# Kernel optimization log

Measured on AMD Instinct MI355X. Metric: run time of the kernel, lower is better.

The kernel has to match this reference:

```python
import jax, jax.numpy as jnp
import numpy as np

WS = 8   # window_size
SS = 4   # shift_size
NH = 8   # num_heads
EPS = 1e-5

def _ln(x, w, b):
    m = jnp.mean(x, axis=-1, keepdims=True)
    v = jnp.var(x, axis=-1, keepdims=True)
    return (x - m) * jax.lax.rsqrt(v + EPS) * w + b

def setup_inputs() -> dict:
    key = jax.random.key(0)
    ks = jax.random.split(key, 6)
    E = 256
    s = 0.02
    return {
        "x": jax.random.normal(ks[0], (8, E, 128, 128), jnp.float32),
        "ln1_w": jnp.ones((E,), jnp.float32),
        "ln1_b": jnp.zeros((E,), jnp.float32),
        "in_proj_w": jax.random.normal(ks[1], (3 * E, E), jnp.float32) * s,
        "in_proj_b": jnp.zeros((3 * E,), jnp.float32),
        "out_proj_w": jax.random.normal(ks[2], (E, E), jnp.float32) * s,
        "out_proj_b": jnp.zeros((E,), jnp.float32),
        "ln2_w": jnp.ones((E,), jnp.float32),
        "ln2_b": jnp.zeros((E,), jnp.float32),
        "mlp_w1": jax.random.normal(ks[3], (4 * E, E), jnp.float32) * s,
        "mlp_b1": jnp.zeros((4 * E,), jnp.float32),
        "mlp_w2": jax.random.normal(ks[4], (E, 4 * E), jnp.float32) * s,
        "mlp_b2": jnp.zeros((E,), jnp.float32),
    }

def reference(x, ln1_w, ln1_b, in_proj_w, in_proj_b, out_proj_w, out_proj_b,
              ln2_w, ln2_b, mlp_w1, mlp_b1, mlp_w2, mlp_b2):
    B, C, H, W = x.shape
    dh = C // NH
    # NCHW -> NHWC, cyclic shift
    xh = jnp.transpose(x, (0, 2, 3, 1))
    xh = jnp.roll(xh, (-SS, -SS), axis=(1, 2))
    # window partition: [B*nWh*nWw, WS*WS, C]
    nWh, nWw = H // WS, W // WS
    win = xh.reshape(B, nWh, WS, nWw, WS, C).transpose(0, 1, 3, 2, 4, 5)
    win = win.reshape(-1, WS * WS, C)
    h = _ln(win, ln1_w, ln1_b)
    qkv = h @ in_proj_w.T + in_proj_b                       # [N, 64, 3C]
    q, k, v = jnp.split(qkv, 3, axis=-1)
    N, T, _ = q.shape
    q = q.reshape(N, T, NH, dh).transpose(0, 2, 1, 3)       # [N, NH, T, dh]
    k = k.reshape(N, T, NH, dh).transpose(0, 2, 1, 3)
    v = v.reshape(N, T, NH, dh).transpose(0, 2, 1, 3)
    scores = jnp.einsum('nhqd,nhkd->nhqk', q, k) / jnp.sqrt(jnp.float32(dh))
    attn = jax.nn.softmax(scores, axis=-1)
    o = jnp.einsum('nhqk,nhkd->nhqd', attn, v)
    o = o.transpose(0, 2, 1, 3).reshape(N, T, C)
    o = o @ out_proj_w.T + out_proj_b
    win = win + o
    # MLP
    h2 = _ln(win, ln2_w, ln2_b)
    m = jax.nn.gelu(h2 @ mlp_w1.T + mlp_b1, approximate=False)
    m = m @ mlp_w2.T + mlp_b2
    win = win + m
    # window reverse + unshift
    xh = win.reshape(B, nWh, nWw, WS, WS, C).transpose(0, 1, 3, 2, 4, 5)
    xh = xh.reshape(B, H, W, C)
    xh = jnp.roll(xh, (SS, SS), axis=(1, 2))
    return jnp.transpose(xh, (0, 3, 1, 2))
```

## Files before the change

### kernel.cpp

```cpp
#include <hip/hip_runtime.h>
#include <math.h>


#define LDH 264
#define LDS_S 40

typedef __attribute__((ext_vector_type(8))) short bf16x8;
typedef __attribute__((ext_vector_type(4))) short bf16x4;
typedef __attribute__((ext_vector_type(4))) float f32x4;

#define WF(wf, tile, KT, kt, ln) (*(const bf16x8*)&(wf)[((((tile)*(KT)) + (kt))*64 + (ln))*8])
#define FRAG(basep, ttile, KT, kt, l) (*(const bf16x8*)&(basep)[((((ttile)*(KT)) + (kt))*64 + (l))*8])

static __device__ __forceinline__ float bf2f(short s){
  union { unsigned u; float f; } cv;
  cv.u = ((unsigned)(unsigned short)s) << 16;
  return cv.f;
}
static __device__ __forceinline__ short f2bf(float f){
  __bf16 h = (__bf16)f;
  union { __bf16 b; short s; } cv; cv.b = h;
  return cv.s;
}
static __device__ __forceinline__ unsigned pk2bf(float lo, float hi){
  return (unsigned)(unsigned short)f2bf(lo) | ((unsigned)(unsigned short)f2bf(hi) << 16);
}
static __device__ __forceinline__ float gelu_f(float x){
  const float x2 = x * x;
  const float u  = x * fmaf(0.0713537014f, x2, 1.5957691216f);
  const float e  = __expf(u);
  const float r  = __builtin_amdgcn_rcpf(e + 1.f);
  return x * (1.f - r);
}

__global__ void wpack_kernel(const float* __restrict__ src, short* __restrict__ dst,
                             int K){
  const int t8 = blockIdx.x * 256 + threadIdx.x;
  const int e0 = t8 * 8;
  const int l   = (e0 >> 3) & 63;
  const int blk = e0 >> 9;
  const int KT  = K >> 5;
  const int kt   = blk % KT;
  const int tile = blk / KT;
  const int row = tile*16 + (l & 15);
  const int kb  = kt*32 + (l >> 4)*8;
  const float* s = src + row*K + kb;
  bf16x8 o;
  #pragma unroll
  for (int e=0;e<8;++e) o[e] = f2bf(s[e]);
  *(bf16x8*)&dst[e0] = o;
}

#define K1_OFF_WV  33792
#define K1_OFF_RED 74752
#define K1_SMEM    76800

__global__ __launch_bounds__(256, 2)
void swin_attn_kernel(const float* __restrict__ x,
                      const float* __restrict__ ln1w, const float* __restrict__ ln1b,
                      const float* __restrict__ inb,  const float* __restrict__ outb,
                      const short* __restrict__ wqkv, const short* __restrict__ wout,
                      short* __restrict__ win2T)
{
  __shared__ char smem[K1_SMEM];
  short* shf    = (short*)smem;
  short* sh_o   = (short*)smem;
  short* xsh    = (short*)(smem + K1_OFF_WV);
  float* red_s  = (float*)(smem + K1_OFF_RED);
  float* red_q2 = red_s + 256;

  const int tid = threadIdx.x;
  const int wv  = tid >> 6;
  const int ln  = tid & 63;
  const int rowa = ln & 15;
  const int kg   = ln >> 4;

  short* slotA = (short*)(smem + K1_OFF_WV) + wv*5120;
  short* slotB = slotA + 2560;

  const int bid = blockIdx.x;
  const int wi  = ((bid & 7) << 8) | (bid >> 3);
  const int b  = wi >> 8;
  const int wh = (wi >> 4) & 15;
  const int ww = wi & 15;

  const int hh = (wh*8 + (ln >> 3) + 4) & 127;
  const int wc = (ww*8 + (ln & 7) + 4) & 127;
  const int offhw = hh*128 + wc;
  const int xbase = b << 22;

  unsigned xpk[32];
  {
    const int cbeg = wv*64;
    float vals[64];
    float s = 0.f, sq = 0.f;
    #pragma unroll
    for (int j = 0; j < 64; ++j){
      float v = x[xbase + ((cbeg + j) << 14) + offhw];
      vals[j] = v; s += v; sq += v*v;
    }
    #pragma unroll
    for (int p = 0; p < 32; ++p)
      xpk[p] = pk2bf(vals[2*p], vals[2*p+1]);
    red_s[cbeg + ln]  = s;
    red_q2[cbeg + ln] = sq;
    __syncthreads();
    float sum = red_s[ln] + red_s[64+ln] + red_s[128+ln] + red_s[192+ln];
    float ssq = red_q2[ln] + red_q2[64+ln] + red_q2[128+ln] + red_q2[192+ln];
    float mean = sum * 0.00390625f;
    float var  = ssq * 0.00390625f - mean*mean;
    float rstd = rsqrtf(var + 1e-5f);
    const int ttile = ln >> 4;
    #pragma unroll
    for (int kl=0;kl<2;++kl){
      const int kt = wv*2 + kl;
      #pragma unroll
      for (int kgw=0;kgw<4;++kgw){
        bf16x8 pkv;
        #pragma unroll
        for (int e=0;e<8;++e){
          const int j = kl*32 + kgw*8 + e;
          const int c = cbeg + j;
          pkv[e] = f2bf((vals[j] - mean) * rstd * ln1w[c] + ln1b[c]);
        }
        *(bf16x8*)&shf[(((ttile*8 + kt)*64) + kgw*16 + (ln & 15))*8] = pkv;
      }
    }
  }
  __syncthreads();

  const float scale = 0.1767766952966369f;
  f32x4 oacc[4][4];
  #pragma unroll
  for (int mt=0;mt<4;++mt)
    #pragma unroll
    for (int j=0;j<4;++j)
      oacc[mt][j] = (f32x4){0.f,0.f,0.f,0.f};

  const int s0 = ((kg & 1) << 5) + rowa;

  #pragma unroll
  for (int hd = 0; hd < 2; ++hd){
    const int hc = (2*wv + hd) * 32;
    const int tq = (2*wv + hd) * 2;

    {
      f32x4 aq[4][2], ak[4][2];
      #pragma unroll
      for (int mt=0;mt<4;++mt){
        aq[mt][0]=(f32x4){0,0,0,0}; aq[mt][1]=(f32x4){0,0,0,0};
        ak[mt][0]=(f32x4){0,0,0,0}; ak[mt][1]=(f32x4){0,0,0,0};
      }
      #pragma unroll
      for (int kt=0;kt<8;++kt){
        bf16x8 av[4], bq[2], bk[2];
        #pragma unroll
        for (int mt=0;mt<4;++mt)
          av[mt] = FRAG(shf, mt, 8, kt, ln);
        #pragma unroll
        for (int nt=0;nt<2;++nt){
          bq[nt] = WF(wqkv, tq + nt,      8, kt, ln);
          bk[nt] = WF(wqkv, 16 + tq + nt, 8, kt, ln);
        }
        #pragma unroll
        for (int mt=0;mt<4;++mt)
          #pragma unroll
          for (int nt=0;nt<2;++nt){
            aq[mt][nt] = __builtin_amdgcn_mfma_f32_16x16x32_bf16(av[mt], bq[nt], aq[mt][nt], 0, 0, 0);
            ak[mt][nt] = __builtin_amdgcn_mfma_f32_16x16x32_bf16(av[mt], bk[nt], ak[mt][nt], 0, 0, 0);
          }
      }
      #pragma unroll
      for (int nt=0;nt<2;++nt){
        const float biasq = inb[hc + nt*16 + rowa];
        const float biask = inb[256 + hc + nt*16 + rowa];
        #pragma unroll
        for (int mt=0;mt<4;++mt)
          #pragma unroll
          for (int i=0;i<4;++i){
            slotA[(mt*16 + kg*4 + i)*LDS_S + nt*16 + rowa] = f2bf(aq[mt][nt][i] + biasq);
            slotB[(mt*16 + kg*4 + i)*LDS_S + nt*16 + rowa] = f2bf(ak[mt][nt][i] + biask);
          }
      }
    }

    f32x4 sacc[4][4];
    #pragma unroll
    for (int mt=0;mt<4;++mt)
      #pragma unroll
      for (int nt=0;nt<4;++nt)
        sacc[mt][nt] = (f32x4){0.f,0.f,0.f,0.f};
    {
      bf16x8 aq[4], bk[4];
      #pragma unroll
      for (int mt=0;mt<4;++mt)
        aq[mt] = *(const bf16x8*)&slotA[(mt*16+rowa)*LDS_S + kg*8];
      #pragma unroll
      for (int nt=0;nt<4;++nt)
        bk[nt] = *(const bf16x8*)&slotB[(nt*16+rowa)*LDS_S + kg*8];
      __builtin_amdgcn_s_setprio(1);
      #pragma unroll
      for (int mt=0;mt<4;++mt)
        #pragma unroll
        for (int nt=0;nt<4;++nt)
          sacc[mt][nt] = __builtin_amdgcn_mfma_f32_16x16x32_bf16(aq[mt], bk[nt], sacc[mt][nt], 0, 0, 0);
      __builtin_amdgcn_s_setprio(0);
    }

    unsigned pkv[4][2][2];
    {
      f32x4 accv[4][2];
      #pragma unroll
      for (int mt=0;mt<4;++mt){ accv[mt][0]=(f32x4){0,0,0,0}; accv[mt][1]=(f32x4){0,0,0,0}; }
      #pragma unroll
      for (int kt=0;kt<8;++kt){
        bf16x8 av[4], bw[2];
        #pragma unroll
        for (int mt=0;mt<4;++mt)
          av[mt] = FRAG(shf, mt, 8, kt, ln);
        #pragma unroll
        for (int nt=0;nt<2;++nt)
          bw[nt] = WF(wqkv, 32 + tq + nt, 8, kt, ln);
        #pragma unroll
        for (int mt=0;mt<4;++mt)
          #pragma unroll
          for (int nt=0;nt<2;++nt)
            accv[mt][nt] = __builtin_amdgcn_mfma_f32_16x16x32_bf16(av[mt], bw[nt], accv[mt][nt], 0, 0, 0);
      }
      #pragma unroll
      for (int nt=0;nt<2;++nt){
        const float bias = inb[512 + hc + nt*16 + rowa];
        #pragma unroll
        for (int mt=0;mt<4;++mt){
          pkv[mt][nt][0] = pk2bf(accv[mt][nt][0] + bias, accv[mt][nt][1] + bias);
          pkv[mt][nt][1] = pk2bf(accv[mt][nt][2] + bias, accv[mt][nt][3] + bias);
        }
      }
    }

    #pragma unroll
    for (int mt=0;mt<4;++mt){
      #pragma unroll
      for (int i=0;i<4;++i){
        float v0 = sacc[mt][0][i]*scale;
        float v1 = sacc[mt][1][i]*scale;
        float v2 = sacc[mt][2][i]*scale;
        float v3 = sacc[mt][3][i]*scale;
        float mx = fmaxf(fmaxf(v0,v1), fmaxf(v2,v3));
        #pragma unroll
        for (int d=1; d<16; d<<=1) mx = fmaxf(mx, __shfl_xor(mx, d, 64));
        v0 = __expf(v0-mx); v1 = __expf(v1-mx); v2 = __expf(v2-mx); v3 = __expf(v3-mx);
        float sm = v0+v1+v2+v3;
        #pragma unroll
        for (int d=1; d<16; d<<=1) sm += __shfl_xor(sm, d, 64);
        const float inv = 1.f / sm;
        sacc[mt][0][i] = v0*inv; sacc[mt][1][i] = v1*inv;
        sacc[mt][2][i] = v2*inv; sacc[mt][3][i] = v3*inv;
      }
    }

    #pragma unroll
    for (int ck=0; ck<2; ++ck){
      #pragma unroll
      for (int ntl=0; ntl<2; ++ntl)
        #pragma unroll
        for (int mt=0;mt<4;++mt)
          #pragma unroll
          for (int i=0;i<4;++i)
            slotA[(mt*16 + kg*4 + i)*LDS_S + ntl*16 + rowa] = f2bf(sacc[mt][2*ck+ntl][i]);
      bf16x8 bv[2];
      #pragma unroll
      for (int nt=0;nt<2;++nt){
        union { unsigned u[4]; bf16x8 v; } bb;
        #pragma unroll
        for (int dh2=0; dh2<2; ++dh2){
          #pragma unroll
          for (int w=0; w<2; ++w){
            const unsigned pe = (unsigned)__shfl((int)pkv[2*ck    ][nt][w], s0 + dh2*16);
            const unsigned po = (unsigned)__shfl((int)pkv[2*ck + 1][nt][w], s0 + dh2*16);
            bb.u[dh2*2 + w] = (kg & 2) ? po : pe;
          }
        }
        bv[nt] = bb.v;
      }
      bf16x8 ap[4];
      #pragma unroll
      for (int mt=0;mt<4;++mt)
        ap[mt] = *(const bf16x8*)&slotA[(mt*16+rowa)*LDS_S + kg*8];
      __builtin_amdgcn_s_setprio(1);
      #pragma unroll
      for (int mt=0;mt<4;++mt)
        #pragma unroll
        for (int nt=0;nt<2;++nt)
          oacc[mt][hd*2+nt] = __builtin_amdgcn_mfma_f32_16x16x32_bf16(ap[mt], bv[nt], oacc[mt][hd*2+nt], 0, 0, 0);
      __builtin_amdgcn_s_setprio(0);
    }
  }

  __syncthreads();

  #pragma unroll
  for (int j=0;j<4;++j){
    const int col = wv*64 + j*16 + rowa;
    #pragma unroll
    for (int mt=0;mt<4;++mt)
      #pragma unroll
      for (int i=0;i<4;++i)
        sh_o[(mt*16 + kg*4 + i)*LDH + col] = f2bf(oacc[mt][j][i]);
  }
  {
    const int cbeg = wv*64;
    #pragma unroll
    for (int q=0;q<8;++q){
      bf16x8 pk;
      #pragma unroll
      for (int e=0;e<4;++e){
        const unsigned w = xpk[q*4+e];
        pk[2*e]   = (short)(w & 0xffffu);
        pk[2*e+1] = (short)(w >> 16);
      }
      *(bf16x8*)&xsh[ln*LDH + cbeg + q*8] = pk;
    }
  }
  __syncthreads();

  {
    f32x4 acc[4][4];
    #pragma unroll
    for (int c0=0;c0<4;++c0)
      #pragma unroll
      for (int t0=0;t0<4;++t0)
        acc[c0][t0] = (f32x4){0.f,0.f,0.f,0.f};
    for (int kt=0; kt<8; ++kt){
      bf16x8 aw[4], bo[4];
      #pragma unroll
      for (int c0=0;c0<4;++c0)
        aw[c0] = WF(wout, wv*4 + c0, 8, kt, ln);
      #pragma unroll
      for (int t0=0;t0<4;++t0)
        bo[t0] = *(const bf16x8*)&sh_o[(t0*16+rowa)*LDH + kt*32 + kg*8];
      #pragma unroll
      for (int c0=0;c0<4;++c0)
        #pragma unroll
        for (int t0=0;t0<4;++t0)
          acc[c0][t0] = __builtin_amdgcn_mfma_f32_16x16x32_bf16(aw[c0], bo[t0], acc[c0][t0], 0, 0, 0);
    }
    #pragma unroll
    for (int c0=0;c0<4;++c0){
      #pragma unroll
      for (int i=0;i<4;++i){
        const int ch = wv*64 + c0*16 + kg*4 + i;
        const float bias = outb[ch];
        #pragma unroll
        for (int t0=0;t0<4;++t0){
          const int tok = t0*16 + rowa;
          const float res = bf2f(xsh[tok*LDH + ch]);
          win2T[(wi<<14) + ch*64 + tok] = f2bf(acc[c0][t0][i] + bias + res);
        }
      }
    }
  }
}

#define K2_OFF_M   32768
#define K2_OFF_RED 49152
#define K2_SMEM    51200

__device__ __forceinline__ void g1h_pre(const bf16x8 aw, const short* Yf,
                                        int kt, int ln, f32x4 acc1[4]){
  bf16x8 bh[4];
  #pragma unroll
  for (int ct=0;ct<4;++ct)
    bh[ct] = FRAG(Yf, ct, 8, kt, ln);
  #pragma unroll
  for (int ct=0;ct<4;++ct)
    acc1[ct] = __builtin_amdgcn_mfma_f32_16x16x32_bf16(aw, bh[ct], acc1[ct], 0, 0, 0);
}

__device__ __forceinline__ void g2h_pre(const short* Mfb, const bf16x8* w2c4,
                                        int kt2, int ln, f32x4 acc2[4][4]){
  bf16x8 bm[4];
  #pragma unroll
  for (int t0=0;t0<4;++t0)
    bm[t0] = FRAG(Mfb, t0, 2, kt2, ln);
  #pragma unroll
  for (int c0=0;c0<4;++c0)
    #pragma unroll
    for (int t0=0;t0<4;++t0)
      acc2[c0][t0] = __builtin_amdgcn_mfma_f32_16x16x32_bf16(w2c4[c0], bm[t0], acc2[c0][t0], 0, 0, 0);
}

__device__ __forceinline__ void gelu_pack(const float* __restrict__ b1p,
                                          const f32x4 acc1[4], bf16x4 stv[4]){
  const f32x4 b1v = *(const f32x4*)b1p;
  #pragma unroll
  for (int ct=0;ct<4;++ct){
    #pragma unroll
    for (int i=0;i<4;++i)
      stv[ct][i] = f2bf(gelu_f(acc1[ct][i] + b1v[i]));
  }
}

__device__ __forceinline__ void st_stv(short* Mfb, int wv, int rowa, int kg,
                                       const bf16x4 stv[4]){
  #pragma unroll
  for (int ct=0;ct<4;++ct)
    *(bf16x4*)&Mfb[(((ct*2 + (wv>>1))*64) + ((wv&1)*2 + (kg>>1))*16 + rowa)*8 + (kg&1)*4] = stv[ct];
}

__global__ __launch_bounds__(256, 3)
void swin_mlp_kernel(const short* __restrict__ win2T,
                     const float* __restrict__ ln2w, const float* __restrict__ ln2b,
                     const float* __restrict__ b1,   const float* __restrict__ b2,
                     const short* __restrict__ w1,   const short* __restrict__ w2,
                     float* __restrict__ out)
{
  __shared__ char smem[K2_SMEM];
  short* Yf  = (short*)smem;
  short* Mf0 = (short*)(smem + K2_OFF_M);
  short* Mf1 = Mf0 + 4096;
  float* red_s  = (float*)(smem + K2_OFF_RED);
  float* red_q2 = red_s + 256;

  const int tid = threadIdx.x;
  const int wv  = tid >> 6;
  const int ln  = tid & 63;
  const int rowa = ln & 15;
  const int kg   = ln >> 4;

  const int bid = blockIdx.x;
  const int wi  = ((bid & 7) << 8) | (bid >> 3);
  const int wb = wi << 14;

  {
    float vals[64];
    float s = 0.f, sq = 0.f;
    const int cbeg = wv*64;
    #pragma unroll
    for (int j=0;j<64;++j){
      float v = bf2f(win2T[wb + (cbeg + j)*64 + ln]);
      vals[j] = v; s += v; sq += v*v;
    }
    red_s[cbeg + ln]  = s;
    red_q2[cbeg + ln] = sq;
    __syncthreads();
    float sum = red_s[ln] + red_s[64+ln] + red_s[128+ln] + red_s[192+ln];
    float ssq = red_q2[ln] + red_q2[64+ln] + red_q2[128+ln] + red_q2[192+ln];
    float mean = sum * 0.00390625f;
    float var  = ssq * 0.00390625f - mean*mean;
    float rstd = rsqrtf(var + 1e-5f);
    const int ttile = ln >> 4;
    #pragma unroll
    for (int kl=0;kl<2;++kl){
      const int kt = wv*2 + kl;
      #pragma unroll
      for (int kgw=0;kgw<4;++kgw){
        bf16x8 pkv;
        #pragma unroll
        for (int e=0;e<8;++e){
          const int j = kl*32 + kgw*8 + e;
          const int c = cbeg + j;
          pkv[e] = f2bf((vals[j] - mean) * rstd * ln2w[c] + ln2b[c]);
        }
        *(bf16x8*)&Yf[(((ttile*8 + kt)*64) + kgw*16 + (ln & 15))*8] = pkv;
      }
    }
  }
  __syncthreads();

  f32x4 acc2[4][4];
  #pragma unroll
  for (int c0=0;c0<4;++c0)
    #pragma unroll
    for (int t0=0;t0<4;++t0)
      acc2[c0][t0] = (f32x4){0.f,0.f,0.f,0.f};

  bf16x4 stv[4];
  {
    f32x4 acc1[4];
    #pragma unroll
    for (int ct=0;ct<4;++ct) acc1[ct] = (f32x4){0.f,0.f,0.f,0.f};
    #pragma unroll
    for (int kt=0;kt<8;++kt)
      g1h_pre(WF(w1, 0*4 + wv, 8, kt, ln), Yf, kt, ln, acc1);
    gelu_pack(&b1[wv*16 + kg*4], acc1, stv);
  }

  bf16x8 w1c[4];
  #pragma unroll
  for (int c = 0; c < 16; ++c){
    short* cur = (c & 1) ? Mf1 : Mf0;
    st_stv(cur, wv, rowa, kg, stv);

    bf16x8 w2c[8];
    #pragma unroll
    for (int j=0;j<8;++j)
      w2c[j] = WF(w2, wv*4 + (j & 3), 32, c*2 + (j >> 2), ln);
    if (c < 15){
      #pragma unroll
      for (int kt=0;kt<4;++kt)
        w1c[kt] = WF(w1, (c+1)*4 + wv, 8, kt, ln);
    }
    __syncthreads();

    if (c < 15){
      f32x4 acc1n[4];
      #pragma unroll
      for (int ct=0;ct<4;++ct) acc1n[ct] = (f32x4){0.f,0.f,0.f,0.f};
      #pragma unroll
      for (int kt=0;kt<4;++kt) g1h_pre(w1c[kt], Yf, kt, ln, acc1n);
      g2h_pre(cur, &w2c[0], 0, ln, acc2);
      #pragma unroll
      for (int kt=4;kt<8;++kt)
        g1h_pre(WF(w1, (c+1)*4 + wv, 8, kt, ln), Yf, kt, ln, acc1n);
      gelu_pack(&b1[(c+1)*64 + wv*16 + kg*4], acc1n, stv);
      g2h_pre(cur, &w2c[4], 1, ln, acc2);
    } else {
      g2h_pre(cur, &w2c[0], 0, ln, acc2);
      g2h_pre(cur, &w2c[4], 1, ln, acc2);
    }
  }

  const int b  = wi >> 8;
  const int wh = (wi >> 4) & 15;
  const int ww = wi & 15;
  #pragma unroll
  for (int c0=0;c0<4;++c0){
    #pragma unroll
    for (int i=0;i<4;++i){
      const int ch = wv*64 + c0*16 + kg*4 + i;
      const float bias = b2[ch];
      #pragma unroll
      for (int t0=0;t0<4;++t0){
        const int tok = t0*16 + rowa;
        float v = acc2[c0][t0][i] + bias + bf2f(win2T[wb + ch*64 + tok]);
        const int r = tok >> 3, cw = tok & 7;
        const int hh = (wh*8 + r + 4) & 127;
        const int wcc = (ww*8 + cw + 4) & 127;
        out[(((b<<8) + ch) << 14) + hh*128 + wcc] = v;
      }
    }
  }
}

extern "C" void kernel_launch(void* const* d_in, const int* in_sizes, int n_in,
                              void* d_out, int out_size, void* d_ws, size_t ws_size,
                              hipStream_t stream) {
  (void)in_sizes; (void)n_in; (void)out_size; (void)ws_size;
  const float* x    = (const float*)d_in[0];
  const float* ln1w = (const float*)d_in[1];
  const float* ln1b = (const float*)d_in[2];
  const float* inw  = (const float*)d_in[3];
  const float* inb  = (const float*)d_in[4];
  const float* outw = (const float*)d_in[5];
  const float* outb = (const float*)d_in[6];
  const float* ln2w = (const float*)d_in[7];
  const float* ln2b = (const float*)d_in[8];
  const float* w1f  = (const float*)d_in[9];
  const float* b1   = (const float*)d_in[10];
  const float* w2f  = (const float*)d_in[11];
  const float* b2   = (const float*)d_in[12];
  float* out = (float*)d_out;

  short* ws    = (short*)d_ws;
  short* wqkv  = ws;
  short* wout  = ws + 196608;
  short* w1b   = ws + 262144;
  short* w2b   = ws + 524288;
  short* win2T = ws + 786432;

  hipLaunchKernelGGL(wpack_kernel, dim3(96),  dim3(256), 0, stream, inw,  wqkv, 256);
  hipLaunchKernelGGL(wpack_kernel, dim3(32),  dim3(256), 0, stream, outw, wout, 256);
  hipLaunchKernelGGL(wpack_kernel, dim3(128), dim3(256), 0, stream, w1f,  w1b,  256);
  hipLaunchKernelGGL(wpack_kernel, dim3(128), dim3(256), 0, stream, w2f,  w2b,  1024);

  hipLaunchKernelGGL(swin_attn_kernel, dim3(2048), dim3(256), 0, stream,
                     x, ln1w, ln1b, inb, outb, wqkv, wout, win2T);
  hipLaunchKernelGGL(swin_mlp_kernel, dim3(2048), dim3(256), 0, stream,
                     win2T, ln2w, ln2b, b1, b2, w1b, w2b, out);
}
```

Before: 392.1 us.

## Compute transposed attention scores to keep softmax probabilities in registers

The score MFMA now produces S^T (keys × queries), so each lane holds a query column. Softmax reduces across registers with only two cross-lane shuffles instead of four per row. The probabilities are packed to bf16 and redistributed by shuffles rather than round-tripping through LDS, and P·V is computed as V^T·P^T. The transposed output accumulators are then written to shared memory as 4-wide vector stores. This removes LDS stores and loads plus scalar stores in the attention loop, at the cost of more shuffle traffic and register pressure.

```diff
diff --git a/kernel.cpp b/kernel.cpp
--- a/kernel.cpp
+++ b/kernel.cpp
@@ -130,12 +130,12 @@
   __syncthreads();
 
   const float scale = 0.1767766952966369f;
-  f32x4 oacc[4][4];
-  #pragma unroll
-  for (int mt=0;mt<4;++mt)
-    #pragma unroll
-    for (int j=0;j<4;++j)
-      oacc[mt][j] = (f32x4){0.f,0.f,0.f,0.f};
+  f32x4 oaccT[4][4];
+  #pragma unroll
+  for (int c=0;c<4;++c)
+    #pragma unroll
+    for (int t=0;t<4;++t)
+      oaccT[c][t] = (f32x4){0.f,0.f,0.f,0.f};
 
   const int s0 = ((kg & 1) << 5) + rowa;
 
@@ -186,24 +186,24 @@
 
     f32x4 sacc[4][4];
     #pragma unroll
-    for (int mt=0;mt<4;++mt)
-      #pragma unroll
-      for (int nt=0;nt<4;++nt)
-        sacc[mt][nt] = (f32x4){0.f,0.f,0.f,0.f};
+    for (int mtk=0;mtk<4;++mtk)
+      #pragma unroll
+      for (int ntq=0;ntq<4;++ntq)
+        sacc[mtk][ntq] = (f32x4){0.f,0.f,0.f,0.f};
     {
-      bf16x8 aq[4], bk[4];
-      #pragma unroll
-      for (int mt=0;mt<4;++mt)
-        aq[mt] = *(const bf16x8*)&slotA[(mt*16+rowa)*LDS_S + kg*8];
-      #pragma unroll
-      for (int nt=0;nt<4;++nt)
-        bk[nt] = *(const bf16x8*)&slotB[(nt*16+rowa)*LDS_S + kg*8];
+      bf16x8 akf[4], bqf[4];
+      #pragma unroll
+      for (int mtk=0;mtk<4;++mtk)
+        akf[mtk] = *(const bf16x8*)&slotB[(mtk*16+rowa)*LDS_S + kg*8];
+      #pragma unroll
+      for (int ntq=0;ntq<4;++ntq)
+        bqf[ntq] = *(const bf16x8*)&slotA[(ntq*16+rowa)*LDS_S + kg*8];
       __builtin_amdgcn_s_setprio(1);
       #pragma unroll
-      for (int mt=0;mt<4;++mt)
-        #pragma unroll
-        for (int nt=0;nt<4;++nt)
-          sacc[mt][nt] = __builtin_amdgcn_mfma_f32_16x16x32_bf16(aq[mt], bk[nt], sacc[mt][nt], 0, 0, 0);
+      for (int mtk=0;mtk<4;++mtk)
+        #pragma unroll
+        for (int ntq=0;ntq<4;++ntq)
+          sacc[mtk][ntq] = __builtin_amdgcn_mfma_f32_16x16x32_bf16(akf[mtk], bqf[ntq], sacc[mtk][ntq], 0, 0, 0);
       __builtin_amdgcn_s_setprio(0);
     }
 
@@ -239,60 +239,76 @@
     }
 
     #pragma unroll
-    for (int mt=0;mt<4;++mt){
-      #pragma unroll
-      for (int i=0;i<4;++i){
-        float v0 = sacc[mt][0][i]*scale;
-        float v1 = sacc[mt][1][i]*scale;
-        float v2 = sacc[mt][2][i]*scale;
-        float v3 = sacc[mt][3][i]*scale;
-        float mx = fmaxf(fmaxf(v0,v1), fmaxf(v2,v3));
-        #pragma unroll
-        for (int d=1; d<16; d<<=1) mx = fmaxf(mx, __shfl_xor(mx, d, 64));
-        v0 = __expf(v0-mx); v1 = __expf(v1-mx); v2 = __expf(v2-mx); v3 = __expf(v3-mx);
-        float sm = v0+v1+v2+v3;
-        #pragma unroll
-        for (int d=1; d<16; d<<=1) sm += __shfl_xor(sm, d, 64);
-        const float inv = 1.f / sm;
-        sacc[mt][0][i] = v0*inv; sacc[mt][1][i] = v1*inv;
-        sacc[mt][2][i] = v2*inv; sacc[mt][3][i] = v3*inv;
-      }
+    for (int ntq=0;ntq<4;++ntq){
+      float mx = sacc[0][ntq][0]*scale;
+      #pragma unroll
+      for (int mtk=0;mtk<4;++mtk)
+        #pragma unroll
+        for (int i=0;i<4;++i)
+          mx = fmaxf(mx, sacc[mtk][ntq][i]*scale);
+      mx = fmaxf(mx, __shfl_xor(mx, 16, 64));
+      mx = fmaxf(mx, __shfl_xor(mx, 32, 64));
+      float sm = 0.f;
+      #pragma unroll
+      for (int mtk=0;mtk<4;++mtk)
+        #pragma unroll
+        for (int i=0;i<4;++i){
+          const float e = __expf(sacc[mtk][ntq][i]*scale - mx);
+          sacc[mtk][ntq][i] = e; sm += e;
+        }
+      sm += __shfl_xor(sm, 16, 64);
+      sm += __shfl_xor(sm, 32, 64);
+      const float inv = 1.f / sm;
+      #pragma unroll
+      for (int mtk=0;mtk<4;++mtk)
+        #pragma unroll
+        for (int i=0;i<4;++i)
+          sacc[mtk][ntq][i] *= inv;
     }
 
     #pragma unroll
     for (int ck=0; ck<2; ++ck){
-      #pragma unroll
-      for (int ntl=0; ntl<2; ++ntl)
-        #pragma unroll
-        for (int mt=0;mt<4;++mt)
-          #pragma unroll
-          for (int i=0;i<4;++i)
-            slotA[(mt*16 + kg*4 + i)*LDS_S + ntl*16 + rowa] = f2bf(sacc[mt][2*ck+ntl][i]);
-      bf16x8 bv[2];
-      #pragma unroll
-      for (int nt=0;nt<2;++nt){
+      unsigned pp[2][4][2];
+      #pragma unroll
+      for (int mm=0;mm<2;++mm)
+        #pragma unroll
+        for (int ntq=0;ntq<4;++ntq){
+          pp[mm][ntq][0] = pk2bf(sacc[2*ck+mm][ntq][0], sacc[2*ck+mm][ntq][1]);
+          pp[mm][ntq][1] = pk2bf(sacc[2*ck+mm][ntq][2], sacc[2*ck+mm][ntq][3]);
+        }
+      bf16x8 avv[2];
+      #pragma unroll
+      for (int c=0;c<2;++c){
         union { unsigned u[4]; bf16x8 v; } bb;
         #pragma unroll
         for (int dh2=0; dh2<2; ++dh2){
           #pragma unroll
           for (int w=0; w<2; ++w){
-            const unsigned pe = (unsigned)__shfl((int)pkv[2*ck    ][nt][w], s0 + dh2*16);
-            const unsigned po = (unsigned)__shfl((int)pkv[2*ck + 1][nt][w], s0 + dh2*16);
+            const unsigned pe = (unsigned)__shfl((int)pkv[2*ck    ][c][w], s0 + dh2*16);
+            const unsigned po = (unsigned)__shfl((int)pkv[2*ck + 1][c][w], s0 + dh2*16);
             bb.u[dh2*2 + w] = (kg & 2) ? po : pe;
           }
         }
-        bv[nt] = bb.v;
-      }
-      bf16x8 ap[4];
-      #pragma unroll
-      for (int mt=0;mt<4;++mt)
-        ap[mt] = *(const bf16x8*)&slotA[(mt*16+rowa)*LDS_S + kg*8];
+        avv[c] = bb.v;
+      }
+      bf16x8 bpf[4];
+      #pragma unroll
+      for (int ntq=0;ntq<4;++ntq){
+        union { unsigned u[4]; bf16x8 v; } bb;
+        #pragma unroll
+        for (int d=0; d<4; ++d){
+          const unsigned pe = (unsigned)__shfl((int)pp[0][ntq][d & 1], s0 + (d>>1)*16);
+          const unsigned po = (unsigned)__shfl((int)pp[1][ntq][d & 1], s0 + (d>>1)*16);
+          bb.u[d] = (kg & 2) ? po : pe;
+        }
+        bpf[ntq] = bb.v;
+      }
       __builtin_amdgcn_s_setprio(1);
       #pragma unroll
-      for (int mt=0;mt<4;++mt)
-        #pragma unroll
-        for (int nt=0;nt<2;++nt)
-          oacc[mt][hd*2+nt] = __builtin_amdgcn_mfma_f32_16x16x32_bf16(ap[mt], bv[nt], oacc[mt][hd*2+nt], 0, 0, 0);
+      for (int c=0;c<2;++c)
+        #pragma unroll
+        for (int ntq=0;ntq<4;++ntq)
+          oaccT[hd*2+c][ntq] = __builtin_amdgcn_mfma_f32_16x16x32_bf16(avv[c], bpf[ntq], oaccT[hd*2+c][ntq], 0, 0, 0);
       __builtin_amdgcn_s_setprio(0);
     }
   }
@@ -300,13 +316,15 @@
   __syncthreads();
 
   #pragma unroll
-  for (int j=0;j<4;++j){
-    const int col = wv*64 + j*16 + rowa;
-    #pragma unroll
-    for (int mt=0;mt<4;++mt)
-      #pragma unroll
-      for (int i=0;i<4;++i)
-        sh_o[(mt*16 + kg*4 + i)*LDH + col] = f2bf(oacc[mt][j][i]);
+  for (int c=0;c<4;++c){
+    const int chb = wv*64 + c*16 + kg*4;
+    #pragma unroll
+    for (int t=0;t<4;++t){
+      bf16x4 st;
+      #pragma unroll
+      for (int i=0;i<4;++i) st[i] = f2bf(oaccT[c][t][i]);
+      *(bf16x4*)&sh_o[(t*16 + rowa)*LDH + chb] = st;
+    }
   }
   {
     const int cbeg = wv*64;
```

New measurement: 358.0 us. -8.7%, faster.
